# Kernel optimization log

Hardware: AMD Instinct MI355X
Metric: run time of the kernel (lower is better)

The kernel has to match this reference:

```python
import jax, jax.numpy as jnp
import numpy as np

B, Q, C, K = 2, 300, 80, 300
MH = MW = 128
TH = TW = 320


def setup_inputs() -> dict:
    key = jax.random.key(0)
    k1, k2, k3 = jax.random.split(key, 3)
    pred_logits = jax.random.normal(k1, (B, Q, C), dtype=jnp.float32)
    pred_boxes = jax.random.uniform(k2, (B, Q, 4), dtype=jnp.float32)  # cxcywh in [0,1]
    pred_masks = jax.random.normal(k3, (B, Q, MH, MW), dtype=jnp.float32)
    # fixed target size so resize output shape is static (original uses .item() per image)
    orig_target_sizes = jnp.full((B, 2), 320.0, dtype=jnp.float32)  # (w, h)
    return {
        'pred_logits': pred_logits,
        'pred_boxes': pred_boxes,
        'pred_masks': pred_masks,
        'orig_target_sizes': orig_target_sizes,
        'target_h': TH,
        'target_w': TW,
    }


def reference(pred_logits, pred_boxes, pred_masks, orig_target_sizes, target_h, target_w):
    b, q, c = pred_logits.shape
    # cxcywh -> xyxy
    cx, cy, w, h = jnp.split(pred_boxes, 4, axis=-1)
    boxes_xyxy = jnp.concatenate([cx - 0.5 * w, cy - 0.5 * h, cx + 0.5 * w, cy + 0.5 * h], axis=-1)
    # scale factor [w, h, w, h] per image
    scale_fct = jnp.concatenate([orig_target_sizes, orig_target_sizes], axis=1)[:, None, :]  # [B,1,4]
    boxes_abs = boxes_xyxy * scale_fct  # [B,Q,4]

    # focal-loss path: sigmoid scores, topk over flattened (query, class)
    scores_flat = jax.nn.sigmoid(pred_logits).reshape(b, q * c)
    scores, index_flat = jax.lax.top_k(scores_flat, K)  # [B,K]
    labels = index_flat % c
    query_indices = index_flat // c  # [B,K]

    top_boxes = jnp.take_along_axis(boxes_abs, query_indices[:, :, None], axis=1)  # [B,K,4]
    top_masks = jnp.take_along_axis(pred_masks, query_indices[:, :, None, None], axis=1)  # [B,K,MH,MW]

    # bilinear resize, half-pixel centers == torch align_corners=False
    resized = jax.image.resize(top_masks, (b, K, target_h, target_w), method='linear')
    binary_masks = (jax.nn.sigmoid(resized) > 0.5).astype(jnp.float32)

    return scores, labels, top_boxes, binary_masks
```

## Files before the change

### kernel.cpp

```cpp
#include <hip/hip_runtime.h>
#include <stdint.h>

constexpr int Bq = 2;
constexpr int Qn = 300;
constexpr int Cn = 80;
constexpr int Kn = 300;
constexpr int NFLAT = Qn * Cn;
constexpr int MHs = 128;
constexpr int MWs = 128;
constexpr int THs = 320;
constexpr int TWs = 320;

constexpr int OFF_SCORES = 0;
constexpr int OFF_LABELS = Bq * Kn;
constexpr int OFF_BOXES  = 2 * Bq * Kn;
constexpr int OFF_MASKS  = 2 * Bq * Kn + Bq * Kn * 4;

typedef float vf4  __attribute__((ext_vector_type(4)));
typedef float uvf4 __attribute__((ext_vector_type(4), aligned(4)));

constexpr size_t WS_GHIST = 0;
constexpr size_t WS_CNT   = 2048;
constexpr size_t WS_THR   = 2064;
constexpr size_t WS_ZERO_BYTES = 2072;
constexpr size_t WS_CAND  = 4096;
constexpr size_t WS_QIDX  = 20480;

__global__ __launch_bounds__(256) void tk_hist(
    const float* __restrict__ logits, int* __restrict__ ghist)
{
    const int b = blockIdx.y;
    __shared__ int lh[256];
    lh[threadIdx.x] = 0;
    __syncthreads();
    const float* lg = logits + (size_t)b * NFLAT;
    #pragma unroll
    for (int j = 0; j < 2; ++j) {
        int idx = blockIdx.x * 512 + j * 256 + threadIdx.x;
        if (idx < NFLAT) {
            float x = lg[idx];
            int bin = min(max((int)floorf((x + 8.0f) * 16.0f), 0), 255);
            atomicAdd(&lh[bin], 1);
        }
    }
    __syncthreads();
    int v = lh[threadIdx.x];
    if (v) atomicAdd(&ghist[b * 256 + threadIdx.x], v);
}

__global__ __launch_bounds__(64) void tk_thresh(
    const int* __restrict__ ghist, int* __restrict__ thr)
{
    const int b = blockIdx.x;
    if (threadIdx.x == 0) {
        int cum = 0, t = 0;
        for (int d = 255; d >= 0; --d) {
            cum += ghist[b * 256 + d];
            if (cum >= Kn) { t = d; break; }
        }
        thr[b] = t;
    }
}

__global__ __launch_bounds__(256) void tk_collect(
    const float* __restrict__ logits, const int* __restrict__ thr,
    int* __restrict__ cnt, unsigned long long* __restrict__ cand)
{
    const int b = blockIdx.y;
    const int T = thr[b];
    const float* lg = logits + (size_t)b * NFLAT;
    #pragma unroll
    for (int j = 0; j < 2; ++j) {
        int idx = blockIdx.x * 512 + j * 256 + threadIdx.x;
        if (idx < NFLAT) {
            float x = lg[idx];
            int bin = min(max((int)floorf((x + 8.0f) * 16.0f), 0), 255);
            if (bin >= T) {
                float s = 1.0f / (1.0f + expf(-x));
                int p = atomicAdd(&cnt[b], 1);
                if (p < 1024)
                    cand[b * 1024 + p] =
                        ((unsigned long long)__float_as_uint(s) << 32)
                      | (unsigned long long)(0xFFFFFFFFu - (uint32_t)idx);
            }
        }
    }
}

__global__ __launch_bounds__(1024) void tk_rank(
    const int* __restrict__ cnt, const unsigned long long* __restrict__ cand,
    const float* __restrict__ boxes, const float* __restrict__ osz,
    float* __restrict__ out, int* __restrict__ qidx_ws)
{
    const int b   = blockIdx.x;
    const int tid = threadIdx.x;
    __shared__ unsigned long long sk[1024];
    const int n = min(cnt[b], 1024);
    sk[tid] = (tid < n) ? cand[b * 1024 + tid] : 0ull;
    __syncthreads();

    if (tid < n) {
        unsigned long long my = sk[tid];
        int rank = 0;
        for (int i = 0; i < n; ++i) rank += (sk[i] > my) ? 1 : 0;
        if (rank < Kn) {
            uint32_t idx = 0xFFFFFFFFu - (uint32_t)(my & 0xFFFFFFFFull);
            float score  = __uint_as_float((uint32_t)(my >> 32));
            int label = (int)(idx % (uint32_t)Cn);
            int q     = (int)(idx / (uint32_t)Cn);

            out[OFF_SCORES + b * Kn + rank] = score;
            out[OFF_LABELS + b * Kn + rank] = (float)label;

            const float sw = osz[b * 2 + 0];
            const float sh = osz[b * 2 + 1];
            const float* bx = boxes + ((size_t)(b * Qn + q)) * 4;
            float cx = bx[0], cy = bx[1], w = bx[2], h = bx[3];
            float* ob = out + OFF_BOXES + ((size_t)(b * Kn + rank)) * 4;
            ob[0] = (cx - 0.5f * w) * sw;
            ob[1] = (cy - 0.5f * h) * sh;
            ob[2] = (cx + 0.5f * w) * sw;
            ob[3] = (cy + 0.5f * h) * sh;

            qidx_ws[b * Kn + rank] = q;
        }
    }
}

__global__ __launch_bounds__(320) void resize_kernel(
    const float* __restrict__ masks,
    const int* __restrict__ qidx_ws,
    float* __restrict__ out)
{
    const int blk = blockIdx.x;
    const int bk  = blk >> 2;
    const int s   = blk & 3;
    const int tid = threadIdx.x;
    const int b   = bk / Kn;
    const int q   = qidx_ws[bk];
    const int c   = tid % 80;
    const int rs  = tid / 80;

    const float* M = masks + ((size_t)(b * Qn + q)) * (MHs * MWs);

    int s0;
    {
        float sx0 = fmaf(0.4f, (float)(4 * c), -0.3f);
        int i0 = (int)floorf(sx0);
        s0 = min(max(i0, 0), MWs - 4);
    }
    float W[4][4];
    #pragma unroll
    for (int t = 0; t < 4; ++t) {
        int ox = 4 * c + t;
        float sx = fmaf(0.4f, (float)ox, -0.3f);
        int ix0 = (int)floorf(sx);
        float fr = sx - (float)ix0;
        int ca = max(ix0, 0);
        int cb = min(ix0 + 1, MWs - 1);
        float wa = 1.0f - fr, wb = fr;
        #pragma unroll
        for (int j = 0; j < 4; ++j) {
            float w = 0.0f;
            if (s0 + j == ca) w += wa;
            if (s0 + j == cb) w += wb;
            W[t][j] = w;
        }
    }

    auto hrow = [&](float* hv, int r) {
        uvf4 a = *(const uvf4*)(M + r * MWs + s0);
        #pragma unroll
        for (int t = 0; t < 4; ++t)
            hv[t] = fmaf(W[t][0], a[0],
                    fmaf(W[t][1], a[1],
                    fmaf(W[t][2], a[2], W[t][3] * a[3])));
    };

    float* outm = out + OFF_MASKS + (size_t)bk * (THs * TWs);
    auto emit = [&](int row, float wA, const float* pA, float wB, const float* pB) {
        vf4 o;
        #pragma unroll
        for (int t = 0; t < 4; ++t) {
            float v = fmaf(wA, pA[t], wB * pB[t]);
            o[t] = (v > 0.0f) ? 1.0f : 0.0f;
        }
        *(vf4*)(outm + (size_t)row * TWs + 4 * c) = o;
    };

    const int Y0 = 80 * s + 20 * rs;
    const int M0 = Y0 / 5;

    float hA[4], hB[4], hC[4], hD[4];
    hrow(hC, max(2 * M0 - 1, 0));
    hrow(hD, 2 * M0);

    #pragma unroll
    for (int g = 0; g < 4; ++g) {
        #pragma unroll
        for (int t = 0; t < 4; ++t) { hA[t] = hC[t]; hB[t] = hD[t]; }
        const int Mg = M0 + g;
        hrow(hC, 2 * Mg + 1);
        hrow(hD, min(2 * Mg + 2, MHs - 1));

        const int Y = Y0 + 5 * g;
        emit(Y + 0, 0.3f, hA, 0.7f, hB);
        emit(Y + 1, 0.9f, hB, 0.1f, hC);
        emit(Y + 2, 0.5f, hB, 0.5f, hC);
        emit(Y + 3, 0.1f, hB, 0.9f, hC);
        emit(Y + 4, 0.7f, hC, 0.3f, hD);
    }
}

extern "C" void kernel_launch(void* const* d_in, const int* in_sizes, int n_in,
                              void* d_out, int out_size, void* d_ws, size_t ws_size,
                              hipStream_t stream) {
    const float* logits = (const float*)d_in[0];
    const float* boxes  = (const float*)d_in[1];
    const float* masks  = (const float*)d_in[2];
    const float* osz    = (const float*)d_in[3];

    float* out = (float*)d_out;
    char* ws = (char*)d_ws;
    int* ghist = (int*)(ws + WS_GHIST);
    int* cnt   = (int*)(ws + WS_CNT);
    int* thr   = (int*)(ws + WS_THR);
    unsigned long long* cand = (unsigned long long*)(ws + WS_CAND);
    int* qidx  = (int*)(ws + WS_QIDX);

    hipMemsetAsync(ws, 0, WS_ZERO_BYTES, stream);

    dim3 g47(47, Bq);
    tk_hist<<<g47, 256, 0, stream>>>(logits, ghist);
    tk_thresh<<<Bq, 64, 0, stream>>>(ghist, thr);
    tk_collect<<<g47, 256, 0, stream>>>(logits, thr, cnt, cand);
    tk_rank<<<Bq, 1024, 0, stream>>>(cnt, cand, boxes, osz, out, qidx);
    resize_kernel<<<Bq * Kn * 4, 320, 0, stream>>>(masks, qidx, out);
}
```

Before: 345.7 us.

## Restructure mask resize as grid-stride sweep and aggregate top-k candidates in LDS

The resize kernel becomes a persistent grid-stride sweep in which each thread computes one float4 of output in flat order, so stores are fully contiguous across the grid. Query indices and horizontal weights are precomputed into shared memory once per block. In exchange, the vertical reuse of horizontally interpolated rows is dropped, so each output needs two fresh row loads and recomputed horizontal taps. Separately, tk_collect buffers candidates in shared memory and does one global atomic per block instead of one per candidate.

Result: no change. 345.2 us (-0.1%).

```diff
diff --git a/kernel.cpp b/kernel.cpp
--- a/kernel.cpp
+++ b/kernel.cpp
@@ -68,6 +68,10 @@
 {
     const int b = blockIdx.y;
     const int T = thr[b];
+    __shared__ unsigned long long lbuf[512];
+    __shared__ int lcnt, lbase;
+    if (threadIdx.x == 0) lcnt = 0;
+    __syncthreads();
     const float* lg = logits + (size_t)b * NFLAT;
     #pragma unroll
     for (int j = 0; j < 2; ++j) {
@@ -77,13 +81,19 @@
             int bin = min(max((int)floorf((x + 8.0f) * 16.0f), 0), 255);
             if (bin >= T) {
                 float s = 1.0f / (1.0f + expf(-x));
-                int p = atomicAdd(&cnt[b], 1);
-                if (p < 1024)
-                    cand[b * 1024 + p] =
-                        ((unsigned long long)__float_as_uint(s) << 32)
-                      | (unsigned long long)(0xFFFFFFFFu - (uint32_t)idx);
+                int p = atomicAdd(&lcnt, 1);
+                if (p < 512)
+                    lbuf[p] = ((unsigned long long)__float_as_uint(s) << 32)
+                            | (unsigned long long)(0xFFFFFFFFu - (uint32_t)idx);
             }
         }
+    }
+    __syncthreads();
+    if (threadIdx.x == 0) lcnt = min(lcnt, 512), lbase = atomicAdd(&cnt[b], lcnt);
+    __syncthreads();
+    for (int i = threadIdx.x; i < lcnt; i += 256) {
+        int d = lbase + i;
+        if (d < 1024) cand[b * 1024 + d] = lbuf[i];
     }
 }
 
@@ -127,88 +137,92 @@
     }
 }
 
-__global__ __launch_bounds__(320) void resize_kernel(
+constexpr int RS_GRID = 2400;
+constexpr int RS_BLK  = 256;
+constexpr int RS_THREADS = RS_GRID * RS_BLK;
+constexpr int N4 = Bq * Kn * (THs * TWs / 4);
+constexpr int RS_ITERS = N4 / RS_THREADS;
+
+__global__ __launch_bounds__(256) void resize_sweep(
     const float* __restrict__ masks,
     const int* __restrict__ qidx_ws,
     float* __restrict__ out)
 {
-    const int blk = blockIdx.x;
-    const int bk  = blk >> 2;
-    const int s   = blk & 3;
+    __shared__ int  qlds[Bq * Kn];
+    __shared__ int  s0lds[80];
+    __shared__ vf4  Wlds[4 * 80];
     const int tid = threadIdx.x;
-    const int b   = bk / Kn;
-    const int q   = qidx_ws[bk];
-    const int c   = tid % 80;
-    const int rs  = tid / 80;
-
-    const float* M = masks + ((size_t)(b * Qn + q)) * (MHs * MWs);
-
-    int s0;
-    {
+
+    for (int i = tid; i < Bq * Kn; i += RS_BLK) qlds[i] = qidx_ws[i];
+    if (tid < 80) {
+        const int c = tid;
         float sx0 = fmaf(0.4f, (float)(4 * c), -0.3f);
         int i0 = (int)floorf(sx0);
-        s0 = min(max(i0, 0), MWs - 4);
-    }
-    float W[4][4];
-    #pragma unroll
-    for (int t = 0; t < 4; ++t) {
-        int ox = 4 * c + t;
-        float sx = fmaf(0.4f, (float)ox, -0.3f);
-        int ix0 = (int)floorf(sx);
-        float fr = sx - (float)ix0;
-        int ca = max(ix0, 0);
-        int cb = min(ix0 + 1, MWs - 1);
-        float wa = 1.0f - fr, wb = fr;
+        int s0 = min(max(i0, 0), MWs - 4);
+        s0lds[c] = s0;
         #pragma unroll
-        for (int j = 0; j < 4; ++j) {
-            float w = 0.0f;
-            if (s0 + j == ca) w += wa;
-            if (s0 + j == cb) w += wb;
-            W[t][j] = w;
-        }
-    }
-
-    auto hrow = [&](float* hv, int r) {
-        uvf4 a = *(const uvf4*)(M + r * MWs + s0);
-        #pragma unroll
-        for (int t = 0; t < 4; ++t)
-            hv[t] = fmaf(W[t][0], a[0],
-                    fmaf(W[t][1], a[1],
-                    fmaf(W[t][2], a[2], W[t][3] * a[3])));
-    };
-
-    float* outm = out + OFF_MASKS + (size_t)bk * (THs * TWs);
-    auto emit = [&](int row, float wA, const float* pA, float wB, const float* pB) {
+        for (int t = 0; t < 4; ++t) {
+            int ox = 4 * c + t;
+            float sx = fmaf(0.4f, (float)ox, -0.3f);
+            int ix0 = (int)floorf(sx);
+            float fr = sx - (float)ix0;
+            int ca = max(ix0, 0);
+            int cb = min(ix0 + 1, MWs - 1);
+            float wa = 1.0f - fr, wb = fr;
+            vf4 w;
+            #pragma unroll
+            for (int j = 0; j < 4; ++j) {
+                float v = 0.0f;
+                if (s0 + j == ca) v += wa;
+                if (s0 + j == cb) v += wb;
+                w[j] = v;
+            }
+            Wlds[t * 80 + c] = w;
+        }
+    }
+    __syncthreads();
+
+    const int g = blockIdx.x * RS_BLK + tid;
+    vf4* out4 = (vf4*)(out + OFF_MASKS);
+
+    #pragma unroll 1
+    for (int it = 0; it < RS_ITERS; ++it) {
+        const int f  = it * RS_THREADS + g;
+        const int bk = f / 25600;
+        const int p  = f - bk * 25600;
+        const int oy = p / 80;
+        const int og = p - oy * 80;
+
+        const int m  = oy / 5;
+        const int ph = oy - 5 * m;
+        int rA = 2 * m + ((ph == 0) ? -1 : ((ph == 4) ? 1 : 0));
+        int rB = min(rA + 1, MHs - 1);
+        rA = max(rA, 0);
+        const float wA = (ph == 0) ? 0.3f : (ph == 1) ? 0.9f :
+                         (ph == 2) ? 0.5f : (ph == 3) ? 0.1f : 0.7f;
+        const float wB = (ph == 0) ? 0.7f : (ph == 1) ? 0.1f :
+                         (ph == 2) ? 0.5f : (ph == 3) ? 0.9f : 0.3f;
+
+        const int qq = qlds[bk];
+        const int bb = (bk >= Kn) ? 1 : 0;
+        const float* M = masks + ((size_t)(bb * Qn + qq)) * (MHs * MWs);
+        const int s0 = s0lds[og];
+
+        uvf4 aA = *(const uvf4*)(M + rA * MWs + s0);
+        uvf4 aB = *(const uvf4*)(M + rB * MWs + s0);
+
         vf4 o;
         #pragma unroll
         for (int t = 0; t < 4; ++t) {
-            float v = fmaf(wA, pA[t], wB * pB[t]);
+            vf4 w = Wlds[t * 80 + og];
+            float hA = fmaf(w[0], aA[0], fmaf(w[1], aA[1],
+                       fmaf(w[2], aA[2], w[3] * aA[3])));
+            float hB = fmaf(w[0], aB[0], fmaf(w[1], aB[1],
+                       fmaf(w[2], aB[2], w[3] * aB[3])));
+            float v  = fmaf(wA, hA, wB * hB);
             o[t] = (v > 0.0f) ? 1.0f : 0.0f;
         }
-        *(vf4*)(outm + (size_t)row * TWs + 4 * c) = o;
-    };
-
-    const int Y0 = 80 * s + 20 * rs;
-    const int M0 = Y0 / 5;
-
-    float hA[4], hB[4], hC[4], hD[4];
-    hrow(hC, max(2 * M0 - 1, 0));
-    hrow(hD, 2 * M0);
-
-    #pragma unroll
-    for (int g = 0; g < 4; ++g) {
-        #pragma unroll
-        for (int t = 0; t < 4; ++t) { hA[t] = hC[t]; hB[t] = hD[t]; }
-        const int Mg = M0 + g;
-        hrow(hC, 2 * Mg + 1);
-        hrow(hD, min(2 * Mg + 2, MHs - 1));
-
-        const int Y = Y0 + 5 * g;
-        emit(Y + 0, 0.3f, hA, 0.7f, hB);
-        emit(Y + 1, 0.9f, hB, 0.1f, hC);
-        emit(Y + 2, 0.5f, hB, 0.5f, hC);
-        emit(Y + 3, 0.1f, hB, 0.9f, hC);
-        emit(Y + 4, 0.7f, hC, 0.3f, hD);
+        out4[f] = o;
     }
 }
 
@@ -235,5 +249,5 @@
     tk_thresh<<<Bq, 64, 0, stream>>>(ghist, thr);
     tk_collect<<<g47, 256, 0, stream>>>(logits, thr, cnt, cand);
     tk_rank<<<Bq, 1024, 0, stream>>>(cnt, cand, boxes, osz, out, qidx);
-    resize_kernel<<<Bq * Kn * 4, 320, 0, stream>>>(masks, qidx, out);
-}
+    resize_sweep<<<RS_GRID, RS_BLK, 0, stream>>>(masks, qidx, out);
+}
```
